# Optimization experiments

Hardware: AMD Instinct MI355X
Metric: run time of the kernel (lower is better)

## Reference

```python
import jax, jax.numpy as jnp
import numpy as np

B, S, E, H = 2, 2048, 1024, 16
HD = E // H
DFF = 4 * E
LN_EPS = 1e-5


def _layernorm(x, g, b):
    mu = jnp.mean(x, axis=-1, keepdims=True)
    var = jnp.mean(jnp.square(x - mu), axis=-1, keepdims=True)
    return (x - mu) * jax.lax.rsqrt(var + LN_EPS) * g + b


def setup_inputs() -> dict:
    key = jax.random.key(0)
    ks = jax.random.split(key, 6)
    inp = {
        "x": jax.random.normal(ks[0], (B, S, E), jnp.float32),
        "ln1_g": jnp.ones((E,), jnp.float32),
        "ln1_b": jnp.zeros((E,), jnp.float32),
        "ln2_g": jnp.ones((E,), jnp.float32),
        "ln2_b": jnp.zeros((E,), jnp.float32),
        # OptimizedPoincareBallLinear init: randn * 0.1, zero bias
        "w_qkv": jax.random.normal(ks[1], (3 * E, E), jnp.float32) * 0.1,
        "b_qkv": jnp.zeros((3 * E,), jnp.float32),
        "w_ao": jax.random.normal(ks[2], (E, E), jnp.float32) * 0.1,
        "b_ao": jnp.zeros((E,), jnp.float32),
        "w_fc": jax.random.normal(ks[3], (DFF, E), jnp.float32) * 0.1,
        "b_fc": jnp.zeros((DFF,), jnp.float32),
        "w_po": jax.random.normal(ks[4], (E, DFF), jnp.float32) * 0.1,
        "b_po": jnp.zeros((E,), jnp.float32),
    }
    return inp


def reference(x, ln1_g, ln1_b, ln2_g, ln2_b, w_qkv, b_qkv, w_ao, b_ao,
              w_fc, b_fc, w_po, b_po):
    # --- attention branch ---
    h = _layernorm(x, ln1_g, ln1_b)
    qkv = h @ w_qkv.T + b_qkv                       # [B,S,3E]
    qkv = qkv.reshape(B, S, H, 3 * HD).transpose(0, 2, 1, 3)  # [B,H,S,3hd]
    q, k, v = jnp.split(qkv, 3, axis=-1)            # each [B,H,S,hd]
    scores = jnp.einsum('bhqd,bhkd->bhqk', q, k) / jnp.sqrt(
        jnp.asarray(HD, jnp.float32))
    causal = jnp.tril(jnp.ones((S, S), bool))        # attn_bias[:, :, :S, :S]
    scores = jnp.where(causal, scores, jnp.finfo(scores.dtype).min)
    attn_w = jax.nn.softmax(scores, axis=-1)         # dropout p=0.1 inactive (eval)
    attn = jnp.einsum('bhqk,bhkd->bhqd', attn_w, v)  # [B,H,S,hd]
    attn = attn.transpose(0, 2, 1, 3).reshape(B, S, E)
    attn = attn @ w_ao.T + b_ao
    x = x + attn
    # --- MLP branch ---
    h2 = _layernorm(x, ln2_g, ln2_b)
    h2 = h2 @ w_fc.T + b_fc
    h2 = jax.nn.gelu(h2, approximate=True)           # GPT-2 gelu_new
    h2 = h2 @ w_po.T + b_po
    x = x + h2
    return x
```

## Files before the change

### kernel.cpp

```cpp
#include <hip/hip_runtime.h>
#include <cstddef>
#include <cstdint>

#define Bc 2
#define Sc 2048
#define Ec 1024
#define Hc 16
#define HDc 64
#define DFFc 4096
#define ROWS (Bc * Sc)

typedef _Float16 half8v __attribute__((ext_vector_type(8)));
typedef _Float16 half4v __attribute__((ext_vector_type(4)));
typedef float f32x4 __attribute__((ext_vector_type(4)));
typedef _Float16 h16;

__device__ inline void gld_lds16(const void* g, void* l) {
    __builtin_amdgcn_global_load_lds(
        (const __attribute__((address_space(1))) void*)g,
        (__attribute__((address_space(3))) void*)l, 16, 0, 0);
}

__device__ inline float gelu_new(float x) {
    float u = 1.5957691216057308f * fmaf(0.044715f * x * x, x, x);
    return x / (1.0f + __expf(-u));
}

__global__ __launch_bounds__(256) void cvt_kernel(const float* __restrict__ in,
                                                  h16* __restrict__ out, int n) {
    int i = (blockIdx.x * 256 + threadIdx.x) * 4;
    float4 v = *(const float4*)(in + i);
    half4v o;
    o.x = (h16)v.x; o.y = (h16)v.y; o.z = (h16)v.z; o.w = (h16)v.w;
    *(half4v*)(out + i) = o;
}

__device__ inline float block_sum256(float v, float* sb) {
    #pragma unroll
    for (int o = 32; o > 0; o >>= 1) v += __shfl_down(v, o, 64);
    int lane = threadIdx.x & 63, w = threadIdx.x >> 6;
    if (lane == 0) sb[w] = v;
    __syncthreads();
    float r = sb[0] + sb[1] + sb[2] + sb[3];
    __syncthreads();
    return r;
}

__global__ __launch_bounds__(256) void ln_kernel(const float* __restrict__ x,
                                                 const float* __restrict__ g,
                                                 const float* __restrict__ b,
                                                 h16* __restrict__ out) {
    __shared__ float sb[4];
    int row = blockIdx.x;
    int t = threadIdx.x;
    const float* xr = x + (size_t)row * Ec;
    float4 v = ((const float4*)xr)[t];
    float s = v.x + v.y + v.z + v.w;
    float mu = block_sum256(s, sb) * (1.0f / Ec);
    float dx = v.x - mu, dy = v.y - mu, dz = v.z - mu, dw = v.w - mu;
    float ss = dx * dx + dy * dy + dz * dz + dw * dw;
    float var = block_sum256(ss, sb) * (1.0f / Ec);
    float inv = rsqrtf(var + 1e-5f);
    float4 gv = ((const float4*)g)[t];
    float4 bv = ((const float4*)b)[t];
    half4v o;
    o.x = (h16)(dx * inv * gv.x + bv.x);
    o.y = (h16)(dy * inv * gv.y + bv.y);
    o.z = (h16)(dz * inv * gv.z + bv.z);
    o.w = (h16)(dw * inv * gv.w + bv.w);
    ((half4v*)(out + (size_t)row * Ec))[t] = o;
}

template <int EPI, typename OutT>
__global__ __launch_bounds__(256) void gemm_mfma(
    const h16* __restrict__ A, const h16* __restrict__ W,
    const float* __restrict__ bias, const float* __restrict__ R,
    OutT* __restrict__ C, int M, int N, int K)
{
    __shared__ h16 As[2][128 * 32];
    __shared__ h16 Ws[2][128 * 32];

    const int t = threadIdx.x;
    const int lane = t & 63, wv = t >> 6;
    const int wm = wv >> 1, wn = wv & 1;
    const int c15 = lane & 15, q = lane >> 4;
    const int row0 = blockIdx.y * 128, col0 = blockIdx.x * 128;
    const int arow = t >> 2, acol = (t & 3) << 3;

    f32x4 acc[4][4];
    #pragma unroll
    for (int i = 0; i < 4; ++i)
        #pragma unroll
        for (int j = 0; j < 4; ++j)
            acc[i][j] = (f32x4){0.f, 0.f, 0.f, 0.f};

    for (int k0 = 0; k0 < K; k0 += 64) {
        __syncthreads();
        #pragma unroll
        for (int kk = 0; kk < 2; ++kk)
            #pragma unroll
            for (int p = 0; p < 2; ++p) {
                int r = p * 64 + arow;
                gld_lds16(A + (size_t)(row0 + r) * K + k0 + kk * 32 + acol,
                          &As[kk][r * 32 + acol]);
                gld_lds16(W + (size_t)(col0 + r) * K + k0 + kk * 32 + acol,
                          &Ws[kk][r * 32 + acol]);
            }
        __syncthreads();

        #pragma unroll
        for (int kk = 0; kk < 2; ++kk) {
            half8v af[4], bf[4];
            #pragma unroll
            for (int i = 0; i < 4; ++i)
                af[i] = *(const half8v*)&As[kk][(wm * 64 + i * 16 + c15) * 32 + q * 8];
            #pragma unroll
            for (int j = 0; j < 4; ++j)
                bf[j] = *(const half8v*)&Ws[kk][(wn * 64 + j * 16 + c15) * 32 + q * 8];
            #pragma unroll
            for (int i = 0; i < 4; ++i)
                #pragma unroll
                for (int j = 0; j < 4; ++j)
                    acc[i][j] = __builtin_amdgcn_mfma_f32_16x16x32_f16(af[i], bf[j], acc[i][j], 0, 0, 0);
        }
    }

    #pragma unroll
    for (int i = 0; i < 4; ++i) {
        #pragma unroll
        for (int j = 0; j < 4; ++j) {
            int col = col0 + wn * 64 + j * 16 + c15;
            float bv = bias[col];
            #pragma unroll
            for (int r = 0; r < 4; ++r) {
                int row = row0 + wm * 64 + i * 16 + q * 4 + r;
                size_t off = (size_t)row * N + col;
                float v = acc[i][j][r] + bv;
                if (EPI == 1) v += R[off];
                if (EPI == 2) v = gelu_new(v);
                if (sizeof(OutT) == 2) ((h16*)C)[off] = (h16)v;
                else ((float*)C)[off] = v;
            }
        }
    }
}

template <int EPI, typename OutT>
__global__ __launch_bounds__(256) void gemm_k64(
    const h16* __restrict__ A, const h16* __restrict__ W,
    const float* __restrict__ bias, const float* __restrict__ R,
    OutT* __restrict__ C, int M, int N, int K)
{
    __shared__ h16 As[2][64 * 32];
    __shared__ h16 Ws[2][128 * 32];

    const int t = threadIdx.x;
    const int lane = t & 63, wv = t >> 6;
    const int wm = wv >> 1, wn = wv & 1;
    const int c15 = lane & 15, q = lane >> 4;
    const int row0 = blockIdx.y * 64, col0 = blockIdx.x * 128;
    const int arow = t >> 2, acol = (t & 3) << 3;

    f32x4 acc[2][4];
    #pragma unroll
    for (int i = 0; i < 2; ++i)
        #pragma unroll
        for (int j = 0; j < 4; ++j)
            acc[i][j] = (f32x4){0.f, 0.f, 0.f, 0.f};

    for (int k0 = 0; k0 < K; k0 += 64) {
        __syncthreads();
        #pragma unroll
        for (int kk = 0; kk < 2; ++kk) {
            gld_lds16(A + (size_t)(row0 + arow) * K + k0 + kk * 32 + acol,
                      &As[kk][arow * 32 + acol]);
            #pragma unroll
            for (int p = 0; p < 2; ++p) {
                int r = p * 64 + arow;
                gld_lds16(W + (size_t)(col0 + r) * K + k0 + kk * 32 + acol,
                          &Ws[kk][r * 32 + acol]);
            }
        }
        __syncthreads();

        #pragma unroll
        for (int kk = 0; kk < 2; ++kk) {
            half8v af[2], bf[4];
            #pragma unroll
            for (int i = 0; i < 2; ++i)
                af[i] = *(const half8v*)&As[kk][(wm * 32 + i * 16 + c15) * 32 + q * 8];
            #pragma unroll
            for (int j = 0; j < 4; ++j)
                bf[j] = *(const half8v*)&Ws[kk][(wn * 64 + j * 16 + c15) * 32 + q * 8];
            #pragma unroll
            for (int i = 0; i < 2; ++i)
                #pragma unroll
                for (int j = 0; j < 4; ++j)
                    acc[i][j] = __builtin_amdgcn_mfma_f32_16x16x32_f16(af[i], bf[j], acc[i][j], 0, 0, 0);
        }
    }

    #pragma unroll
    for (int i = 0; i < 2; ++i) {
        #pragma unroll
        for (int j = 0; j < 4; ++j) {
            int col = col0 + wn * 64 + j * 16 + c15;
            float bv = bias[col];
            #pragma unroll
            for (int r = 0; r < 4; ++r) {
                int row = row0 + wm * 32 + i * 16 + q * 4 + r;
                size_t off = (size_t)row * N + col;
                float v = acc[i][j][r] + bv;
                if (EPI == 1) v += R[off];
                if (EPI == 2) v = gelu_new(v);
                if (sizeof(OutT) == 2) ((h16*)C)[off] = (h16)v;
                else ((float*)C)[off] = v;
            }
        }
    }
}

__global__ __launch_bounds__(256) void attn_mfma(const h16* __restrict__ qkv,
                                                 h16* __restrict__ attn) {
    __shared__ h16 Ks[2][2][64 * 32];
    __shared__ h16 Vt[2][2][64 * 32];
    __shared__ h16 Ps[4][2][16 * 72];

    const int t = threadIdx.x;
    const int lane = t & 63, wv = t >> 6;
    const int c15 = lane & 15, q = lane >> 4;
    const int bh = blockIdx.y, b = bh >> 4, h = bh & 15;
    const int ja = blockIdx.x;
    const int jb = 31 - ja;
    const int qa0 = ja * 64 + wv * 16;
    const int qb0 = jb * 64 + wv * 16;
    const int ktmax = 31 - ja;

    const int SE = 3 * Ec;
    const size_t hbase = (size_t)b * Sc * SE + (size_t)h * (3 * HDc);

    half8v qfa[2], qfb[2];
    #pragma unroll
    for (int kk = 0; kk < 2; ++kk) {
        qfa[kk] = *(const half8v*)(qkv + hbase + (size_t)(qa0 + c15) * SE + kk * 32 + q * 8);
        qfb[kk] = *(const half8v*)(qkv + hbase + (size_t)(qb0 + c15) * SE + kk * 32 + q * 8);
    }

    f32x4 O[2][4];
    #pragma unroll
    for (int i = 0; i < 2; ++i)
        #pragma unroll
        for (int n = 0; n < 4; ++n)
            O[i][n] = (f32x4){0.f, 0.f, 0.f, 0.f};
    float mi[2] = {-3e38f, -3e38f}, li[2] = {0.f, 0.f};

    const int krow = t >> 2, kjj = t & 3;
    const int vkey = t & 31, vd0 = (t >> 5) << 3;
    half8v vreg[2];

    auto stageK = [&](int kt, int bf) {
        #pragma unroll
        for (int p = 0; p < 2; ++p)
            gld_lds16(qkv + hbase + (size_t)(kt * 64 + krow) * SE + HDc + p * 32 + kjj * 8,
                      &Ks[bf][p][krow * 32 + kjj * 8]);
    };
    auto loadV = [&](int kt) {
        #pragma unroll
        for (int p = 0; p < 2; ++p)
            vreg[p] = *(const half8v*)(qkv + hbase +
                        (size_t)(kt * 64 + p * 32 + vkey) * SE + 2 * HDc + vd0);
    };
    auto scatV = [&](int bf) {
        #pragma unroll
        for (int p = 0; p < 2; ++p)
            #pragma unroll
            for (int u = 0; u < 8; ++u)
                Vt[bf][p][(vd0 + u) * 32 + vkey] = vreg[p][u];
    };

    stageK(0, 0); loadV(0); scatV(0);

    for (int kt = 0; kt <= ktmax; ++kt) {
        const int bf = kt & 1;
        __syncthreads();
        if (kt < ktmax) { stageK(kt + 1, bf ^ 1); loadV(kt + 1); }
        const int k0 = kt * 64;

        half8v kf[4][2];
        #pragma unroll
        for (int j = 0; j < 4; ++j)
            #pragma unroll
            for (int kk = 0; kk < 2; ++kk)
                kf[j][kk] = *(const half8v*)&Ks[bf][kk][(j * 16 + c15) * 32 + q * 8];

        #pragma unroll
        for (int i = 0; i < 2; ++i) {
            if (i == 0 && kt > ja) continue;
            const half8v* qf = i ? qfb : qfa;
            const int qrow = (i ? qb0 : qa0) + c15;

            f32x4 st[4];
            #pragma unroll
            for (int j = 0; j < 4; ++j) {
                f32x4 z = (f32x4){0.f, 0.f, 0.f, 0.f};
                z = __builtin_amdgcn_mfma_f32_16x16x32_f16(kf[j][0], qf[0], z, 0, 0, 0);
                st[j] = __builtin_amdgcn_mfma_f32_16x16x32_f16(kf[j][1], qf[1], st[j] = z, 0, 0, 0);
            }

            float sv[16];
            float mx = mi[i];
            #pragma unroll
            for (int j = 0; j < 4; ++j)
                #pragma unroll
                for (int r = 0; r < 4; ++r) {
                    int key = k0 + j * 16 + q * 4 + r;
                    float v = st[j][r] * 0.125f;
                    v = (key <= qrow) ? v : -3e38f;
                    sv[j * 4 + r] = v;
                    mx = fmaxf(mx, v);
                }
            mx = fmaxf(mx, __shfl_xor(mx, 16, 64));
            mx = fmaxf(mx, __shfl_xor(mx, 32, 64));
            float al = __expf(mi[i] - mx);
            mi[i] = mx;
            float ps = 0.f;
            #pragma unroll
            for (int j = 0; j < 4; ++j)
                #pragma unroll
                for (int r = 0; r < 4; ++r) {
                    float p = __expf(sv[j * 4 + r] - mx);
                    ps += p;
                    Ps[wv][i][c15 * 72 + j * 16 + q * 4 + r] = (h16)p;
                }
            ps += __shfl_xor(ps, 16, 64);
            ps += __shfl_xor(ps, 32, 64);
            li[i] = li[i] * al + ps;

            float alr[4];
            #pragma unroll
            for (int r = 0; r < 4; ++r) alr[r] = __shfl(al, q * 4 + r, 64);
            #pragma unroll
            for (int n = 0; n < 4; ++n)
                #pragma unroll
                for (int r = 0; r < 4; ++r) O[i][n][r] *= alr[r];

            half8v pa0 = *(const half8v*)&Ps[wv][i][c15 * 72 + q * 8];
            half8v pa1 = *(const half8v*)&Ps[wv][i][c15 * 72 + 32 + q * 8];
            #pragma unroll
            for (int n = 0; n < 4; ++n) {
                half8v vf0 = *(const half8v*)&Vt[bf][0][(n * 16 + c15) * 32 + q * 8];
                half8v vf1 = *(const half8v*)&Vt[bf][1][(n * 16 + c15) * 32 + q * 8];
                O[i][n] = __builtin_amdgcn_mfma_f32_16x16x32_f16(pa0, vf0, O[i][n], 0, 0, 0);
                O[i][n] = __builtin_amdgcn_mfma_f32_16x16x32_f16(pa1, vf1, O[i][n], 0, 0, 0);
            }
        }
        if (kt < ktmax) scatV(bf ^ 1);
    }

    #pragma unroll
    for (int i = 0; i < 2; ++i) {
        int qb0i = i ? qb0 : qa0;
        float lr[4];
        #pragma unroll
        for (int r = 0; r < 4; ++r) lr[r] = __shfl(li[i], q * 4 + r, 64);
        #pragma unroll
        for (int r = 0; r < 4; ++r) {
            int row = qb0i + q * 4 + r;
            float rl = 1.0f / lr[r];
            #pragma unroll
            for (int n = 0; n < 4; ++n)
                attn[((size_t)(b * Sc + row)) * Ec + h * HDc + n * 16 + c15] =
                    (h16)(O[i][n][r] * rl);
        }
    }
}

extern "C" void kernel_launch(void* const* d_in, const int* in_sizes, int n_in,
                              void* d_out, int out_size, void* d_ws, size_t ws_size,
                              hipStream_t stream) {
    const float* x     = (const float*)d_in[0];
    const float* ln1_g = (const float*)d_in[1];
    const float* ln1_b = (const float*)d_in[2];
    const float* ln2_g = (const float*)d_in[3];
    const float* ln2_b = (const float*)d_in[4];
    const float* w_qkv = (const float*)d_in[5];
    const float* b_qkv = (const float*)d_in[6];
    const float* w_ao  = (const float*)d_in[7];
    const float* b_ao  = (const float*)d_in[8];
    const float* w_fc  = (const float*)d_in[9];
    const float* b_fc  = (const float*)d_in[10];
    const float* w_po  = (const float*)d_in[11];
    const float* b_po  = (const float*)d_in[12];
    float* out = (float*)d_out;

    char* w = (char*)d_ws;
    h16* wqkv = (h16*)(w);
    h16* wao  = (h16*)(w + 6291456);
    h16* wfc  = (h16*)(w + 8388608);
    h16* wpo  = (h16*)(w + 16777216);
    h16* hb   = (h16*)(w + 25165824);
    h16* qkv  = (h16*)(w + 33554432);
    h16* attn = (h16*)(w + 58720256);
    float* x1 = (float*)(w + 67108864);
    h16* ff   = qkv;

    dim3 blk(256);

    cvt_kernel<<<dim3(3 * Ec * Ec / 1024), blk, 0, stream>>>(w_qkv, wqkv, 3 * Ec * Ec);
    cvt_kernel<<<dim3(Ec * Ec / 1024), blk, 0, stream>>>(w_ao, wao, Ec * Ec);
    cvt_kernel<<<dim3(DFFc * Ec / 1024), blk, 0, stream>>>(w_fc, wfc, DFFc * Ec);
    cvt_kernel<<<dim3(Ec * DFFc / 1024), blk, 0, stream>>>(w_po, wpo, Ec * DFFc);

    ln_kernel<<<dim3(ROWS), blk, 0, stream>>>(x, ln1_g, ln1_b, hb);
    gemm_mfma<0, h16><<<dim3(3 * Ec / 128, ROWS / 128), blk, 0, stream>>>(
        hb, wqkv, b_qkv, nullptr, qkv, ROWS, 3 * Ec, Ec);
    attn_mfma<<<dim3(16, Bc * Hc), blk, 0, stream>>>(qkv, attn);
    gemm_k64<1, float><<<dim3(Ec / 128, ROWS / 64), blk, 0, stream>>>(
        attn, wao, b_ao, x, x1, ROWS, Ec, Ec);
    ln_kernel<<<dim3(ROWS), blk, 0, stream>>>(x1, ln2_g, ln2_b, hb);
    gemm_mfma<2, h16><<<dim3(DFFc / 128, ROWS / 128), blk, 0, stream>>>(
        hb, wfc, b_fc, nullptr, ff, ROWS, DFFc, Ec);
    gemm_k64<1, float><<<dim3(Ec / 128, ROWS / 64), blk, 0, stream>>>(
        ff, wpo, b_po, x1, out, ROWS, Ec, DFFc);
}
```

Before: 379.9 us.

## Restructure causal attention to one query tile per block, heaviest first

Each attention block used to process a pair of query tiles (ja and 31-ja) to balance causal work. Now each block handles a single 64-row query tile, and the grid is ordered so the longest-running tiles launch first. A launch-bounds occupancy hint of 4 blocks is added. The kernel also pre-scales Q by 1/8, applies the causal mask only on the diagonal tile, and swaps the MFMA operand order so outputs are stored as packed half4 vectors. V now uses a single LDS buffer guarded by extra barriers, which cuts LDS use and register pressure but adds synchronisation on every key tile.

```diff
diff --git a/kernel.cpp b/kernel.cpp
--- a/kernel.cpp
+++ b/kernel.cpp
@@ -220,49 +220,42 @@
     }
 }
 
-__global__ __launch_bounds__(256) void attn_mfma(const h16* __restrict__ qkv,
-                                                 h16* __restrict__ attn) {
+__global__ __launch_bounds__(256, 4) void attn_mfma(const h16* __restrict__ qkv,
+                                                    h16* __restrict__ attn) {
     __shared__ h16 Ks[2][2][64 * 32];
-    __shared__ h16 Vt[2][2][64 * 32];
-    __shared__ h16 Ps[4][2][16 * 72];
+    __shared__ h16 Vt[2][64 * 32];
+    __shared__ h16 Ps[4][16 * 72];
 
     const int t = threadIdx.x;
     const int lane = t & 63, wv = t >> 6;
     const int c15 = lane & 15, q = lane >> 4;
-    const int bh = blockIdx.y, b = bh >> 4, h = bh & 15;
-    const int ja = blockIdx.x;
-    const int jb = 31 - ja;
-    const int qa0 = ja * 64 + wv * 16;
-    const int qb0 = jb * 64 + wv * 16;
-    const int ktmax = 31 - ja;
-
+    const int bh = blockIdx.x, b = bh >> 4, h = bh & 15;
+    const int ja = 31 - blockIdx.y;
+    const int qbase = ja * 64 + wv * 16;
     const int SE = 3 * Ec;
     const size_t hbase = (size_t)b * Sc * SE + (size_t)h * (3 * HDc);
 
-    half8v qfa[2], qfb[2];
+    half8v qf[2];
     #pragma unroll
     for (int kk = 0; kk < 2; ++kk) {
-        qfa[kk] = *(const half8v*)(qkv + hbase + (size_t)(qa0 + c15) * SE + kk * 32 + q * 8);
-        qfb[kk] = *(const half8v*)(qkv + hbase + (size_t)(qb0 + c15) * SE + kk * 32 + q * 8);
-    }
-
-    f32x4 O[2][4];
-    #pragma unroll
-    for (int i = 0; i < 2; ++i)
-        #pragma unroll
-        for (int n = 0; n < 4; ++n)
-            O[i][n] = (f32x4){0.f, 0.f, 0.f, 0.f};
-    float mi[2] = {-3e38f, -3e38f}, li[2] = {0.f, 0.f};
-
-    const int krow = t >> 2, kjj = t & 3;
+        qf[kk] = *(const half8v*)(qkv + hbase + (size_t)(qbase + c15) * SE + kk * 32 + q * 8);
+        qf[kk] *= (h16)0.125f;
+    }
+
+    f32x4 O[4];
+    #pragma unroll
+    for (int n = 0; n < 4; ++n) O[n] = (f32x4){0.f, 0.f, 0.f, 0.f};
+    float mi = -3e38f, li = 0.f;
+
+    const int krow = t >> 2, kcol = (t & 3) << 3;
     const int vkey = t & 31, vd0 = (t >> 5) << 3;
     half8v vreg[2];
 
     auto stageK = [&](int kt, int bf) {
         #pragma unroll
         for (int p = 0; p < 2; ++p)
-            gld_lds16(qkv + hbase + (size_t)(kt * 64 + krow) * SE + HDc + p * 32 + kjj * 8,
-                      &Ks[bf][p][krow * 32 + kjj * 8]);
+            gld_lds16(qkv + hbase + (size_t)(kt * 64 + krow) * SE + HDc + p * 32 + kcol,
+                      &Ks[bf][p][krow * 32 + kcol]);
     };
     auto loadV = [&](int kt) {
         #pragma unroll
@@ -270,108 +263,93 @@
             vreg[p] = *(const half8v*)(qkv + hbase +
                         (size_t)(kt * 64 + p * 32 + vkey) * SE + 2 * HDc + vd0);
     };
-    auto scatV = [&](int bf) {
+    auto scatV = [&]() {
         #pragma unroll
         for (int p = 0; p < 2; ++p)
             #pragma unroll
             for (int u = 0; u < 8; ++u)
-                Vt[bf][p][(vd0 + u) * 32 + vkey] = vreg[p][u];
+                Vt[p][(vd0 + u) * 32 + vkey] = vreg[p][u];
     };
 
-    stageK(0, 0); loadV(0); scatV(0);
-
-    for (int kt = 0; kt <= ktmax; ++kt) {
+    stageK(0, 0);
+    loadV(0);
+    scatV();
+    __syncthreads();
+
+    for (int kt = 0; kt <= ja; ++kt) {
         const int bf = kt & 1;
-        __syncthreads();
-        if (kt < ktmax) { stageK(kt + 1, bf ^ 1); loadV(kt + 1); }
-        const int k0 = kt * 64;
-
-        half8v kf[4][2];
-        #pragma unroll
-        for (int j = 0; j < 4; ++j)
-            #pragma unroll
-            for (int kk = 0; kk < 2; ++kk)
-                kf[j][kk] = *(const half8v*)&Ks[bf][kk][(j * 16 + c15) * 32 + q * 8];
-
-        #pragma unroll
-        for (int i = 0; i < 2; ++i) {
-            if (i == 0 && kt > ja) continue;
-            const half8v* qf = i ? qfb : qfa;
-            const int qrow = (i ? qb0 : qa0) + c15;
-
-            f32x4 st[4];
-            #pragma unroll
-            for (int j = 0; j < 4; ++j) {
-                f32x4 z = (f32x4){0.f, 0.f, 0.f, 0.f};
-                z = __builtin_amdgcn_mfma_f32_16x16x32_f16(kf[j][0], qf[0], z, 0, 0, 0);
-                st[j] = __builtin_amdgcn_mfma_f32_16x16x32_f16(kf[j][1], qf[1], st[j] = z, 0, 0, 0);
-            }
-
-            float sv[16];
-            float mx = mi[i];
+        if (kt < ja) { stageK(kt + 1, bf ^ 1); loadV(kt + 1); }
+
+        f32x4 st[4];
+        #pragma unroll
+        for (int j = 0; j < 4; ++j) {
+            half8v kf0 = *(const half8v*)&Ks[bf][0][(j * 16 + c15) * 32 + q * 8];
+            half8v kf1 = *(const half8v*)&Ks[bf][1][(j * 16 + c15) * 32 + q * 8];
+            f32x4 z = (f32x4){0.f, 0.f, 0.f, 0.f};
+            z = __builtin_amdgcn_mfma_f32_16x16x32_f16(kf0, qf[0], z, 0, 0, 0);
+            st[j] = __builtin_amdgcn_mfma_f32_16x16x32_f16(kf1, qf[1], z, 0, 0, 0);
+        }
+
+        if (kt == ja) {
+            const int rowloc = wv * 16 + c15;
             #pragma unroll
             for (int j = 0; j < 4; ++j)
                 #pragma unroll
-                for (int r = 0; r < 4; ++r) {
-                    int key = k0 + j * 16 + q * 4 + r;
-                    float v = st[j][r] * 0.125f;
-                    v = (key <= qrow) ? v : -3e38f;
-                    sv[j * 4 + r] = v;
-                    mx = fmaxf(mx, v);
-                }
-            mx = fmaxf(mx, __shfl_xor(mx, 16, 64));
-            mx = fmaxf(mx, __shfl_xor(mx, 32, 64));
-            float al = __expf(mi[i] - mx);
-            mi[i] = mx;
-            float ps = 0.f;
-            #pragma unroll
-            for (int j = 0; j < 4; ++j)
-                #pragma unroll
-                for (int r = 0; r < 4; ++r) {
-                    float p = __expf(sv[j * 4 + r] - mx);
-                    ps += p;
-                    Ps[wv][i][c15 * 72 + j * 16 + q * 4 + r] = (h16)p;
-                }
-            ps += __shfl_xor(ps, 16, 64);
-            ps += __shfl_xor(ps, 32, 64);
-            li[i] = li[i] * al + ps;
-
-            float alr[4];
-            #pragma unroll
-            for (int r = 0; r < 4; ++r) alr[r] = __shfl(al, q * 4 + r, 64);
-            #pragma unroll
-            for (int n = 0; n < 4; ++n)
-                #pragma unroll
-                for (int r = 0; r < 4; ++r) O[i][n][r] *= alr[r];
-
-            half8v pa0 = *(const half8v*)&Ps[wv][i][c15 * 72 + q * 8];
-            half8v pa1 = *(const half8v*)&Ps[wv][i][c15 * 72 + 32 + q * 8];
-            #pragma unroll
-            for (int n = 0; n < 4; ++n) {
-                half8v vf0 = *(const half8v*)&Vt[bf][0][(n * 16 + c15) * 32 + q * 8];
-                half8v vf1 = *(const half8v*)&Vt[bf][1][(n * 16 + c15) * 32 + q * 8];
-                O[i][n] = __builtin_amdgcn_mfma_f32_16x16x32_f16(pa0, vf0, O[i][n], 0, 0, 0);
-                O[i][n] = __builtin_amdgcn_mfma_f32_16x16x32_f16(pa1, vf1, O[i][n], 0, 0, 0);
+                for (int r = 0; r < 4; ++r)
+                    if (j * 16 + q * 4 + r > rowloc) st[j][r] = -3e38f;
+        }
+
+        float mx = mi;
+        #pragma unroll
+        for (int j = 0; j < 4; ++j)
+            #pragma unroll
+            for (int r = 0; r < 4; ++r) mx = fmaxf(mx, st[j][r]);
+        mx = fmaxf(mx, __shfl_xor(mx, 16, 64));
+        mx = fmaxf(mx, __shfl_xor(mx, 32, 64));
+        float al = __expf(mi - mx);
+        mi = mx;
+        float ps = 0.f;
+        #pragma unroll
+        for (int j = 0; j < 4; ++j) {
+            half4v pk;
+            #pragma unroll
+            for (int r = 0; r < 4; ++r) {
+                float p = __expf(st[j][r] - mx);
+                ps += p;
+                pk[r] = (h16)p;
             }
-        }
-        if (kt < ktmax) scatV(bf ^ 1);
-    }
-
-    #pragma unroll
-    for (int i = 0; i < 2; ++i) {
-        int qb0i = i ? qb0 : qa0;
-        float lr[4];
-        #pragma unroll
-        for (int r = 0; r < 4; ++r) lr[r] = __shfl(li[i], q * 4 + r, 64);
-        #pragma unroll
-        for (int r = 0; r < 4; ++r) {
-            int row = qb0i + q * 4 + r;
-            float rl = 1.0f / lr[r];
-            #pragma unroll
-            for (int n = 0; n < 4; ++n)
-                attn[((size_t)(b * Sc + row)) * Ec + h * HDc + n * 16 + c15] =
-                    (h16)(O[i][n][r] * rl);
-        }
+            *(half4v*)&Ps[wv][c15 * 72 + j * 16 + q * 4] = pk;
+        }
+        ps += __shfl_xor(ps, 16, 64);
+        ps += __shfl_xor(ps, 32, 64);
+        li = li * al + ps;
+
+        half8v pb0 = *(const half8v*)&Ps[wv][c15 * 72 + q * 8];
+        half8v pb1 = *(const half8v*)&Ps[wv][c15 * 72 + 32 + q * 8];
+        #pragma unroll
+        for (int n = 0; n < 4; ++n) {
+            #pragma unroll
+            for (int r = 0; r < 4; ++r) O[n][r] *= al;
+            half8v va0 = *(const half8v*)&Vt[0][(n * 16 + c15) * 32 + q * 8];
+            half8v va1 = *(const half8v*)&Vt[1][(n * 16 + c15) * 32 + q * 8];
+            O[n] = __builtin_amdgcn_mfma_f32_16x16x32_f16(va0, pb0, O[n], 0, 0, 0);
+            O[n] = __builtin_amdgcn_mfma_f32_16x16x32_f16(va1, pb1, O[n], 0, 0, 0);
+        }
+
+        if (kt < ja) {
+            __syncthreads();
+            scatV();
+            __syncthreads();
+        }
+    }
+
+    float rl = 1.0f / li;
+    #pragma unroll
+    for (int n = 0; n < 4; ++n) {
+        half4v o4;
+        #pragma unroll
+        for (int r = 0; r < 4; ++r) o4[r] = (h16)(O[n][r] * rl);
+        *(half4v*)(attn + ((size_t)(b * Sc + qbase + c15)) * Ec + h * HDc + n * 16 + q * 4) = o4;
     }
 }
 
@@ -414,7 +392,7 @@
     ln_kernel<<<dim3(ROWS), blk, 0, stream>>>(x, ln1_g, ln1_b, hb);
     gemm_mfma<0, h16><<<dim3(3 * Ec / 128, ROWS / 128), blk, 0, stream>>>(
         hb, wqkv, b_qkv, nullptr, qkv, ROWS, 3 * Ec, Ec);
-    attn_mfma<<<dim3(16, Bc * Hc), blk, 0, stream>>>(qkv, attn);
+    attn_mfma<<<dim3(Bc * Hc, 32), blk, 0, stream>>>(qkv, attn);
     gemm_k64<1, float><<<dim3(Ec / 128, ROWS / 64), blk, 0, stream>>>(
         attn, wao, b_ao, x, x1, ROWS, Ec, Ec);
     ln_kernel<<<dim3(ROWS), blk, 0, stream>>>(x1, ln2_g, ln2_b, hb);
```

Measured after the change: 364.7 us. 1.04x faster.
